# Performance work log

Hardware: AMD Instinct MI355X
Metric: run time of the kernel (lower is better)

## Reference

```python
import jax, jax.numpy as jnp
import numpy as np

DIM = 128      # d_msa
HEADS = 8
DH = 64        # dim_head
INNER = HEADS * DH  # 512
R = 64         # tie_attn_dim (MSA rows)
N = 512        # residues
DPAIR = 128
LN_EPS = 1e-5


def _layernorm(x, g, b):
    mu = jnp.mean(x, axis=-1, keepdims=True)
    var = jnp.mean((x - mu) ** 2, axis=-1, keepdims=True)
    return (x - mu) * jax.lax.rsqrt(var + LN_EPS) * g + b


def setup_inputs() -> dict:
    key = jax.random.key(0)
    ks = jax.random.split(key, 12)
    s = 0.02
    return {
        "x": jax.random.normal(ks[0], (R, N, DIM), jnp.float32),
        "pair_bias": jax.random.normal(ks[1], (1, N, N, DPAIR), jnp.float32),
        "Wq": jax.random.normal(ks[2], (DIM, INNER), jnp.float32) * s,
        "Wkv": jax.random.normal(ks[3], (DIM, 2 * INNER), jnp.float32) * s,
        "Wo": jax.random.normal(ks[4], (INNER, DIM), jnp.float32) * s,
        "bo": jnp.zeros((DIM,), jnp.float32),
        "ln_g": jnp.ones((DPAIR,), jnp.float32),
        "ln_b": jnp.zeros((DPAIR,), jnp.float32),
        "Wpair": jax.random.normal(ks[5], (DPAIR, HEADS), jnp.float32) * s,
        "Wsq": jax.random.normal(ks[6], (DIM, DIM), jnp.float32) * s,
        "bsq": jnp.zeros((DIM,), jnp.float32),
        "Wsk": jax.random.normal(ks[7], (DIM, DIM), jnp.float32) * s,
        "bsk": jnp.zeros((DIM,), jnp.float32),
        "tie_attn_dim": R,
    }


def reference(x, pair_bias, Wq, Wkv, Wo, bo, ln_g, ln_b, Wpair, Wsq, bsq, Wsk, bsk, tie_attn_dim):
    r = tie_attn_dim
    br, n, dim = x.shape
    b = br // r
    h, dh = HEADS, DH
    dsw = dim // h  # per-head dim inside PositionalWiseWeight

    # projections: (b*r, n, inner) -> (b, r, h, n, dh)
    q = (x @ Wq).reshape(b, r, n, h, dh).transpose(0, 1, 3, 2, 4)
    kv = x @ Wkv
    k, v = jnp.split(kv, 2, axis=-1)
    k = k.reshape(b, r, n, h, dh).transpose(0, 1, 3, 2, 4)
    v = v.reshape(b, r, n, h, dh).transpose(0, 1, 3, 2, 4)

    # soft tied row weights (PositionalWiseWeight): w[b, i(pos), h, r]
    m = x.reshape(b, r, n, dim)
    sq = (m[:, :1] @ Wsq + bsq).reshape(b, 1, n, h, dsw).transpose(0, 2, 3, 1, 4)  # b n h 1 d
    sk = (m @ Wsk + bsk).reshape(b, r, n, h, dsw).transpose(0, 2, 3, 1, 4)          # b n h r d
    wlog = jnp.einsum('bnhud,bnhrd->bnhr', sq, sk) / np.float32(np.sqrt(dsw))
    w = jax.nn.softmax(wlog, axis=-1)  # softmax over rows r

    # tied-row attention logits with soft weights
    scale = np.float32(dh) ** -0.5
    dots = jnp.einsum('bihr,brhid,brhjd->bhij', w, q, k) * scale

    # pair bias: LayerNorm + Linear(dim_pair -> heads), broadcast into logits
    pb = _layernorm(pair_bias, ln_g, ln_b) @ Wpair  # (b, i, j, h)
    dots = dots + pb.transpose(0, 3, 1, 2)

    attn = jax.nn.softmax(dots, axis=-1)  # (b, h, i, j)

    out = jnp.einsum('bhij,brhjd->brhid', attn, v)           # (b, r, h, n, dh)
    out = out.transpose(0, 1, 3, 2, 4).reshape(br, n, h * dh)
    out = out @ Wo + bo                                       # (b*r, n, dim)
    return out.reshape(1, br, n, dim)
```

## Files before the change

kernel.cpp:

```cpp
#include <hip/hip_runtime.h>
#include <hip/hip_bf16.h>

typedef unsigned short u16;
typedef unsigned int u32;
typedef __attribute__((ext_vector_type(8))) short short8;
typedef __attribute__((ext_vector_type(4))) float floatx4;

__device__ inline float bf2f(u16 u) { union { u32 i; float f; } v; v.i = ((u32)u) << 16; return v.f; }
__device__ inline u16 f2bf(float f) {
    union { float f; u32 i; } v; v.f = f;
    u32 lsb = (v.i >> 16) & 1u;
    v.i += 0x7fffu + lsb;
    return (u16)(v.i >> 16);
}

__device__ inline uint4 pack8(float4 a, float4 b) {
    uint4 q;
    q.x = (u32)f2bf(a.x) | ((u32)f2bf(a.y) << 16);
    q.y = (u32)f2bf(a.z) | ((u32)f2bf(a.w) << 16);
    q.z = (u32)f2bf(b.x) | ((u32)f2bf(b.y) << 16);
    q.w = (u32)f2bf(b.z) | ((u32)f2bf(b.w) << 16);
    return q;
}

__device__ inline void ld8(u16* dst, const float* src) {
    const float4 a = *(const float4*)src;
    const float4 b = *(const float4*)(src + 4);
    *(uint4*)dst = pack8(a, b);
}

__device__ inline void async16(u16* ldst, const u16* gsrc) {
    __builtin_amdgcn_global_load_lds((const __attribute__((address_space(1))) u32*)gsrc,
                                     (__attribute__((address_space(3))) u32*)ldst, 16, 0, 0);
}

template <int BM, int BN, class Epi>
__global__ __launch_bounds__(256) void gemm_nt(const u16* __restrict__ A, const u16* __restrict__ B,
                                               long sAz, long sBz, int lda, int ldb, int K, int zlog, Epi epi)
{
    constexpr int AELE = BM * 32, BELE = BN * 32;
    constexpr int IA = BM / 64, IB = BN / 64;
    constexpr bool STAGE = Epi::chunked;
    static_assert(!STAGE || BN == 128, "chunked epilogue assumes BN=128");
    constexpr int LDC = BN + 4;
    constexpr size_t OPB = sizeof(u16) * 2 * (AELE + BELE);
    constexpr size_t STB = STAGE ? sizeof(float) * (size_t)BM * LDC : 0;
    constexpr size_t LB = OPB > STB ? OPB : STB;
    __shared__ __align__(16) char smem[LB];
    u16* lds = (u16*)smem;
    const int tid  = threadIdx.x;
    const int lane = tid & 63;
    const int wave = tid >> 6;
    const int z    = blockIdx.z;
    const int zh   = z >> zlog;
    const int zk   = z & ((1 << zlog) - 1);
    const long row0 = (long)blockIdx.y * BM;
    const long col0 = (long)blockIdx.x * BN;
    const u16* Ab = A + (long)zh * sAz + row0 * lda + (long)zk * K;
    const u16* Bb = B + (long)zh * sBz + col0 * ldb + (long)zk * K;
    constexpr int WM = BM / 2, WN = BN / 2, TM = WM / 16, TN = WN / 16;
    const int wm = (wave >> 1) * WM;
    const int wn = (wave & 1) * WN;
    const int l15 = lane & 15;
    const int quad = lane >> 4;
    const int swz = (l15 >> 1) & 3;

    floatx4 acc[TM][TN];
#pragma unroll
    for (int i = 0; i < TM; i++)
#pragma unroll
        for (int j = 0; j < TN; j++) acc[i][j] = (floatx4){0.f, 0.f, 0.f, 0.f};

    auto stage = [&](int buf, int k0) {
        u16* base = lds + buf * (AELE + BELE);
#pragma unroll
        for (int i = 0; i < IA; i++) {
            int s = wave * (IA * 64) + i * 64 + lane;
            int r = s >> 2, c = (s & 3) ^ ((r >> 1) & 3);
            async16(base + (wave * (IA * 64) + i * 64) * 8, Ab + (long)r * lda + k0 + c * 8);
        }
        u16* bbase = base + AELE;
#pragma unroll
        for (int i = 0; i < IB; i++) {
            int s = wave * (IB * 64) + i * 64 + lane;
            int r = s >> 2, c = (s & 3) ^ ((r >> 1) & 3);
            async16(bbase + (wave * (IB * 64) + i * 64) * 8, Bb + (long)r * ldb + k0 + c * 8);
        }
    };

    stage(0, 0);
    const int nIter = K >> 5;
    for (int ki = 0; ki < nIter; ki++) {
        const int cur = ki & 1;
        __syncthreads();
        if (ki + 1 < nIter) stage(1 - cur, (ki + 1) << 5);
        const u16* As = lds + cur * (AELE + BELE);
        const u16* Bs = As + AELE;
        short8 af[TM], bfr[TN];
#pragma unroll
        for (int t = 0; t < TM; t++)
            af[t] = *(const short8*)(As + (wm + t * 16 + l15) * 32 + (quad ^ swz) * 8);
#pragma unroll
        for (int t = 0; t < TN; t++)
            bfr[t] = *(const short8*)(Bs + (wn + t * 16 + l15) * 32 + (quad ^ swz) * 8);
#pragma unroll
        for (int i = 0; i < TM; i++)
#pragma unroll
            for (int j = 0; j < TN; j++)
                acc[i][j] = __builtin_amdgcn_mfma_f32_16x16x32_bf16(af[i], bfr[j], acc[i][j], 0, 0, 0);
    }

    if constexpr (STAGE) {
        __syncthreads();
        float* cs = (float*)smem;
#pragma unroll
        for (int i = 0; i < TM; i++)
#pragma unroll
            for (int j = 0; j < TN; j++)
#pragma unroll
                for (int r = 0; r < 4; r++)
                    cs[(wm + i * 16 + quad * 4 + r) * LDC + (wn + j * 16 + l15)] = acc[i][j][r];
        __syncthreads();
        constexpr int CPT = (BM * BN) / (256 * 8);
#pragma unroll
        for (int k = 0; k < CPT; k++) {
            int g = k * 256 + tid;
            int row = g >> 4;
            int c8 = (g & 15) * 8;
            const float* p = cs + row * LDC + c8;
            float4 a = *(const float4*)p;
            float4 b = *(const float4*)(p + 4);
            epi.chunk(zh, zk, (int)row0 + row, (int)col0 + c8, a, b);
        }
    } else {
#pragma unroll
        for (int i = 0; i < TM; i++)
#pragma unroll
            for (int j = 0; j < TN; j++)
#pragma unroll
                for (int r = 0; r < 4; r++) {
                    int row = (int)row0 + wm + i * 16 + quad * 4 + r;
                    int col = (int)col0 + wn + j * 16 + l15;
                    epi(zh, zk, row, col, acc[i][j][r]);
                }
    }
}

struct EpiBiasBF {
    static constexpr bool chunked = true;
    u16* C; const float* bias; int ldc;
    __device__ void chunk(int, int, int row, int col, float4 a, float4 b) const {
        const float4* bp = (const float4*)(bias + col);
        float4 b0 = bp[0], b1 = bp[1];
        a.x += b0.x; a.y += b0.y; a.z += b0.z; a.w += b0.w;
        b.x += b1.x; b.y += b1.y; b.z += b1.z; b.w += b1.w;
        *(uint4*)(C + (long)row * ldc + col) = pack8(a, b);
    }
};
struct EpiQ {
    static constexpr bool chunked = true;
    u16* Qw; const float* w;
    __device__ void chunk(int, int, int row, int col, float4 a, float4 b) const {
        int r = row >> 9, i = row & 511, h = col >> 6, d = col & 63;
        float s = w[((long)(i * 8 + h)) * 64 + r] * 0.125f;
        a.x *= s; a.y *= s; a.z *= s; a.w *= s;
        b.x *= s; b.y *= s; b.z *= s; b.w *= s;
        *(uint4*)(Qw + (long)h * 2097152 + (long)i * 4096 + r * 64 + d) = pack8(a, b);
    }
};
struct EpiKV {
    static constexpr bool chunked = true;
    u16* Kp; u16* Vp;
    __device__ void chunk(int, int, int row, int col, float4 a, float4 b) const {
        int r = row >> 9, j = row & 511;
        u16* dst = (col < 512) ? Kp : Vp;
        int c = col & 511;
        int h = c >> 6, d = c & 63;
        *(uint4*)(dst + (long)h * 2097152 + (long)j * 4096 + r * 64 + d) = pack8(a, b);
    }
};
struct EpiDotsAtomic {
    static constexpr bool chunked = false;
    float* pbdots;
    __device__ void operator()(int zh, int, int row, int col, float v) const {
        atomicAdd(pbdots + (long)zh * 262144 + (long)row * 512 + col, v);
    }
};
struct EpiDotsPart {
    static constexpr bool chunked = false;
    float* pbd; float* parts;
    __device__ void operator()(int zh, int zk, int row, int col, float v) const {
        long idx = (long)zh * 262144 + (long)row * 512 + col;
        if (zk == 0) pbd[idx] += v;
        else         parts[(long)(zk - 1) * 2097152 + idx] = v;
    }
};
struct EpiPV {
    static constexpr bool chunked = true;
    u16* O2;
    __device__ void chunk(int zh, int, int row, int col, float4 a, float4 b) const {
        int r = col >> 6, d = col & 63;
        *(uint4*)(O2 + ((long)r * 512 + row) * 512 + zh * 64 + d) = pack8(a, b);
    }
};
struct EpiOut {
    static constexpr bool chunked = true;
    float* out; const float* bo;
    __device__ void chunk(int, int, int row, int col, float4 a, float4 b) const {
        const float4* bp = (const float4*)(bo + col);
        float4 b0 = bp[0], b1 = bp[1];
        a.x += b0.x; a.y += b0.y; a.z += b0.z; a.w += b0.w;
        b.x += b1.x; b.y += b1.y; b.z += b1.z; b.w += b1.w;
        float4* o = (float4*)(out + (long)row * 128 + col);
        o[0] = a; o[1] = b;
    }
};

__global__ __launch_bounds__(256) void f2bf_kernel(const float* __restrict__ src, u16* __restrict__ dst)
{
    long i = ((long)blockIdx.x * 256 + threadIdx.x) * 8;
    ld8(dst + i, src + i);
}

__global__ __launch_bounds__(256) void transpose_to_bf16(const float* __restrict__ src, u16* __restrict__ dst,
                                                         int R, int C)
{
    __shared__ u16 t[32][33];
    int c0 = blockIdx.x * 32, r0 = blockIdx.y * 32;
    int tx = threadIdx.x, ty = threadIdx.y;
#pragma unroll
    for (int i = 0; i < 32; i += 8) t[ty + i][tx] = f2bf(src[(long)(r0 + ty + i) * C + c0 + tx]);
    __syncthreads();
#pragma unroll
    for (int i = 0; i < 32; i += 8) dst[(long)(c0 + ty + i) * R + r0 + tx] = t[tx][ty + i];
}

__global__ __launch_bounds__(256) void transpose64(const u16* __restrict__ src, u16* __restrict__ dst,
                                                   long ss, long ds, int R, int C)
{
    __shared__ __align__(16) u16 t[64][72];
    const u16* s = src + (long)blockIdx.z * ss;
    u16* d = dst + (long)blockIdx.z * ds;
    int c0 = blockIdx.x * 64, r0 = blockIdx.y * 64;
    int tid = threadIdx.x;
    int row = tid >> 3, ch = tid & 7;
#pragma unroll
    for (int p = 0; p < 2; p++) {
        int r = row + p * 32;
        *(uint4*)&t[r][ch * 8] = *(const uint4*)(s + (long)(r0 + r) * C + c0 + ch * 8);
    }
    __syncthreads();
#pragma unroll
    for (int p = 0; p < 2; p++) {
        int cc = row + p * 32;
        u16 tmp[8];
#pragma unroll
        for (int j = 0; j < 8; j++) tmp[j] = t[ch * 8 + j][cc];
        *(uint4*)(d + (long)(c0 + cc) * R + r0 + ch * 8) = *(uint4*)tmp;
    }
}

__global__ __launch_bounds__(256) void rowweight_kernel(const u16* __restrict__ sk, const u16* __restrict__ sq,
                                                        float* __restrict__ w)
{
    int wid = blockIdx.x * 4 + (threadIdx.x >> 6);
    int lane = threadIdx.x & 63;
    int i = wid >> 3, h = wid & 7;
    const u16* sqp = sq + i * 128 + h * 16;
    const u16* skp = sk + ((long)lane * 512 + i) * 128 + h * 16;
    float dot = 0.f;
#pragma unroll
    for (int c = 0; c < 16; c++) dot += bf2f(sqp[c]) * bf2f(skp[c]);
    float logit = dot * 0.25f;
    float m = logit;
#pragma unroll
    for (int o = 32; o > 0; o >>= 1) m = fmaxf(m, __shfl_xor(m, o));
    float e = __expf(logit - m);
    float ssum = e;
#pragma unroll
    for (int o = 32; o > 0; o >>= 1) ssum += __shfl_xor(ssum, o);
    w[(long)wid * 64 + lane] = e / ssum;
}

__global__ __launch_bounds__(256) void pbprep_kernel(const float* __restrict__ g, const float* __restrict__ b,
                                                     const float* __restrict__ Wp, float* __restrict__ Wg,
                                                     float* __restrict__ SB)
{
    int tid = threadIdx.x;
    for (int t = tid; t < 1024; t += 256) Wg[t] = g[t >> 3] * Wp[t];
    if (tid < 16) {
        int h = tid & 7;
        const float* src = (tid < 8) ? g : b;
        float s = 0.f;
        for (int c = 0; c < 128; c++) s += src[c] * Wp[c * 8 + h];
        SB[tid] = s;
    }
}

__global__ __launch_bounds__(256) void pb_kernel(const float* __restrict__ pair, const float* __restrict__ Wg,
                                                 const float* __restrict__ SB, float* __restrict__ pb)
{
    __shared__ __align__(16) float Ls[64 * 132];
    __shared__ float sWg[1024];
    __shared__ float sSB[16];
    int tid = threadIdx.x;
    for (int t = tid; t < 1024; t += 256) sWg[t] = Wg[t];
    if (tid < 16) sSB[tid] = SB[tid];
    long base = (long)blockIdx.x * 8192;
    const float4* src = (const float4*)(pair + base);
#pragma unroll
    for (int k = 0; k < 8; k++) {
        int e = tid + k * 256;
        float4 v = src[e];
        int r = e >> 5, c = (e & 31) << 2;
        *(float4*)(&Ls[r * 132 + c]) = v;
    }
    __syncthreads();
    int r = tid >> 2, sub = tid & 3;
    const float* row = &Ls[r * 132];
    float sum = 0.f, sqs = 0.f;
#pragma unroll
    for (int k = 0; k < 8; k++) {
        float4 v = *(const float4*)(&row[sub * 32 + k * 4]);
        sum += v.x + v.y + v.z + v.w;
        sqs += v.x * v.x + v.y * v.y + v.z * v.z + v.w * v.w;
    }
    sum += __shfl_xor(sum, 1); sqs += __shfl_xor(sqs, 1);
    sum += __shfl_xor(sum, 2); sqs += __shfl_xor(sqs, 2);
    float mu = sum * (1.f / 128.f);
    float var = sqs * (1.f / 128.f) - mu * mu;
    float rstd = rsqrtf(var + 1e-5f);
    int h0 = sub * 2;
    float a0 = 0.f, a1 = 0.f;
#pragma unroll
    for (int k = 0; k < 32; k++) {
        float4 v = *(const float4*)(&row[k * 4]);
        int c = k * 4;
        a0 += v.x * sWg[c * 8 + h0]     + v.y * sWg[(c + 1) * 8 + h0]
            + v.z * sWg[(c + 2) * 8 + h0] + v.w * sWg[(c + 3) * 8 + h0];
        a1 += v.x * sWg[c * 8 + h0 + 1]     + v.y * sWg[(c + 1) * 8 + h0 + 1]
            + v.z * sWg[(c + 2) * 8 + h0 + 1] + v.w * sWg[(c + 3) * 8 + h0 + 1];
    }
    long idx = (long)blockIdx.x * 64 + r;
    pb[(long)h0 * 262144 + idx]       = rstd * (a0 - mu * sSB[h0])     + sSB[8 + h0];
    pb[(long)(h0 + 1) * 262144 + idx] = rstd * (a1 - mu * sSB[h0 + 1]) + sSB[8 + h0 + 1];
}

__global__ __launch_bounds__(256) void softmax_kernel(const float* __restrict__ dots,
                                                      const float* __restrict__ parts, int np,
                                                      u16* __restrict__ attn)
{
    int row = blockIdx.x * 4 + (threadIdx.x >> 6);
    int lane = threadIdx.x & 63;
    long base = (long)row * 512;
    const float* dp = dots + base;
    float v[8];
#pragma unroll
    for (int k = 0; k < 8; k++) v[k] = dp[k * 64 + lane];
    for (int t = 0; t < np; t++) {
        const float* pp = parts + (long)t * 2097152 + base;
#pragma unroll
        for (int k = 0; k < 8; k++) v[k] += pp[k * 64 + lane];
    }
    float m = v[0];
#pragma unroll
    for (int k = 1; k < 8; k++) m = fmaxf(m, v[k]);
#pragma unroll
    for (int o = 32; o > 0; o >>= 1) m = fmaxf(m, __shfl_xor(m, o));
    float s = 0.f;
#pragma unroll
    for (int k = 0; k < 8; k++) { v[k] = __expf(v[k] - m); s += v[k]; }
#pragma unroll
    for (int o = 32; o > 0; o >>= 1) s += __shfl_xor(s, o);
    float inv = 1.f / s;
    u16* ap = attn + (long)row * 512;
#pragma unroll
    for (int k = 0; k < 8; k++) ap[k * 64 + lane] = f2bf(v[k] * inv);
}

extern "C" void kernel_launch(void* const* d_in, const int* in_sizes, int n_in,
                              void* d_out, int out_size, void* d_ws, size_t ws_size,
                              hipStream_t stream)
{
    const float* x    = (const float*)d_in[0];
    const float* pair = (const float*)d_in[1];
    const float* Wq   = (const float*)d_in[2];
    const float* Wkv  = (const float*)d_in[3];
    const float* Wo   = (const float*)d_in[4];
    const float* bo   = (const float*)d_in[5];
    const float* lng  = (const float*)d_in[6];
    const float* lnb  = (const float*)d_in[7];
    const float* Wp   = (const float*)d_in[8];
    const float* Wsq  = (const float*)d_in[9];
    const float* bsq  = (const float*)d_in[10];
    const float* Wsk  = (const float*)d_in[11];
    const float* bsk  = (const float*)d_in[12];
    float* out = (float*)d_out;

    char* ws = (char*)d_ws;
    size_t off = 0;
    auto alloc = [&](size_t bytes) -> char* {
        char* p = ws + off; off += (bytes + 255) & ~(size_t)255; return p;
    };
    u16* WqT  = (u16*)alloc(512 * 128 * 2);
    u16* WkvT = (u16*)alloc(1024 * 128 * 2);
    u16* WskT = (u16*)alloc(128 * 128 * 2);
    u16* WsqT = (u16*)alloc(128 * 128 * 2);
    u16* WoT  = (u16*)alloc(128 * 512 * 2);
    u16* xbf  = (u16*)alloc((size_t)32768 * 128 * 2);
    u16* sk   = (u16*)alloc((size_t)32768 * 128 * 2);
    u16* sq   = (u16*)alloc(512 * 128 * 2);
    float* w  = (float*)alloc((size_t)4096 * 64 * 4);
    float* Wg = (float*)alloc(1024 * 4);
    float* SB = (float*)alloc(16 * 4);
    u16* bufA = (u16*)alloc((size_t)8 * 512 * 4096 * 2);
    u16* bufB = (u16*)alloc((size_t)8 * 512 * 4096 * 2);
    u16* Vt   = (u16*)alloc((size_t)8 * 4096 * 512 * 2);
    float* pbd = (float*)alloc((size_t)8 * 512 * 512 * 4);
    float* parts = (float*)alloc((size_t)3 * 2097152 * 4);
    const bool useParts = (off <= ws_size);
    u16* attn = sk;

    dim3 blk(256);
    dim3 tb(32, 8);

    f2bf_kernel<<<dim3(2048), blk, 0, stream>>>(x, xbf);
    pbprep_kernel<<<dim3(1), blk, 0, stream>>>(lng, lnb, Wp, Wg, SB);

    transpose_to_bf16<<<dim3(16, 4, 1), tb, 0, stream>>>(Wq,  WqT,  128, 512);
    transpose_to_bf16<<<dim3(32, 4, 1), tb, 0, stream>>>(Wkv, WkvT, 128, 1024);
    transpose_to_bf16<<<dim3(4, 4, 1),  tb, 0, stream>>>(Wsk, WskT, 128, 128);
    transpose_to_bf16<<<dim3(4, 4, 1),  tb, 0, stream>>>(Wsq, WsqT, 128, 128);
    transpose_to_bf16<<<dim3(4, 16, 1), tb, 0, stream>>>(Wo,  WoT,  512, 128);

    gemm_nt<64, 128, EpiBiasBF><<<dim3(1, 512, 1), blk, 0, stream>>>(
        xbf, WskT, 0, 0, 128, 128, 128, 0, EpiBiasBF{sk, bsk, 128});
    gemm_nt<64, 128, EpiBiasBF><<<dim3(1, 8, 1), blk, 0, stream>>>(
        xbf, WsqT, 0, 0, 128, 128, 128, 0, EpiBiasBF{sq, bsq, 128});
    rowweight_kernel<<<dim3(1024), blk, 0, stream>>>(sk, sq, w);

    gemm_nt<128, 128, EpiKV><<<dim3(8, 256, 1), blk, 0, stream>>>(
        xbf, WkvT, 0, 0, 128, 128, 128, 0, EpiKV{bufB, bufA});
    transpose64<<<dim3(64, 8, 8), blk, 0, stream>>>(bufA, Vt, 2097152, 2097152, 512, 4096);

    gemm_nt<128, 128, EpiQ><<<dim3(4, 256, 1), blk, 0, stream>>>(
        xbf, WqT, 0, 0, 128, 128, 128, 0, EpiQ{bufA, w});

    pb_kernel<<<dim3(4096), blk, 0, stream>>>(pair, Wg, SB, pbd);

    if (useParts) {
        gemm_nt<128, 128, EpiDotsPart><<<dim3(4, 4, 32), blk, 0, stream>>>(
            bufA, bufB, 2097152, 2097152, 4096, 4096, 1024, 2, EpiDotsPart{pbd, parts});
        softmax_kernel<<<dim3(1024), blk, 0, stream>>>(pbd, parts, 3, attn);
    } else {
        gemm_nt<128, 128, EpiDotsAtomic><<<dim3(4, 4, 64), blk, 0, stream>>>(
            bufA, bufB, 2097152, 2097152, 4096, 4096, 512, 3, EpiDotsAtomic{pbd});
        softmax_kernel<<<dim3(1024), blk, 0, stream>>>(pbd, pbd, 0, attn);
    }

    gemm_nt<128, 128, EpiPV><<<dim3(32, 4, 8), blk, 0, stream>>>(
        attn, Vt, 262144, 2097152, 512, 512, 512, 0, EpiPV{bufB});

    gemm_nt<64, 128, EpiOut><<<dim3(1, 512, 1), blk, 0, stream>>>(
        bufB, WoT, 0, 0, 512, 512, 512, 0, EpiOut{out, bo});
}
```

Measured before the change: 421.0 us.

## Use 4-slot LDS pipeline with explicit vmcnt waits and chunked epilogue staging

Replaces the double-buffered K loop in the generic GEMM with a 4-slot ring that keeps two K-tiles of async global-to-LDS loads in flight. Each step waits with explicit vmcnt counts and a single raw barrier instead of __syncthreads, so load latency can hide behind the MFMA work. The staged epilogue now writes 64 rows at a time, which keeps the LDS footprint near the larger ring buffer, and the pair-bias kernel launch moves ahead of the Q projection. The risks are the hand-written wait counts and a possible loss of occupancy from the larger LDS allocation.

```diff
diff --git a/kernel.cpp b/kernel.cpp
--- a/kernel.cpp
+++ b/kernel.cpp
@@ -34,18 +34,37 @@
                                      (__attribute__((address_space(3))) u32*)ldst, 16, 0, 0);
 }
 
+template <int N> __device__ inline void waitvm() {
+    static_assert(N == 0 || N == 3 || N == 4 || N == 6 || N == 8, "unsupported vmcnt");
+    if constexpr (N == 0) asm volatile("s_waitcnt vmcnt(0)" ::: "memory");
+    if constexpr (N == 3) asm volatile("s_waitcnt vmcnt(3)" ::: "memory");
+    if constexpr (N == 4) asm volatile("s_waitcnt vmcnt(4)" ::: "memory");
+    if constexpr (N == 6) asm volatile("s_waitcnt vmcnt(6)" ::: "memory");
+    if constexpr (N == 8) asm volatile("s_waitcnt vmcnt(8)" ::: "memory");
+}
+__device__ inline void barrier_raw() {
+    asm volatile("s_barrier" ::: "memory");
+    __builtin_amdgcn_sched_barrier(0);
+}
+__device__ inline void waitlgkm0() {
+    asm volatile("s_waitcnt lgkmcnt(0)" ::: "memory");
+    __builtin_amdgcn_sched_barrier(0);
+}
+
 template <int BM, int BN, class Epi>
 __global__ __launch_bounds__(256) void gemm_nt(const u16* __restrict__ A, const u16* __restrict__ B,
                                                long sAz, long sBz, int lda, int ldb, int K, int zlog, Epi epi)
 {
     constexpr int AELE = BM * 32, BELE = BN * 32;
+    constexpr int SLOT = AELE + BELE;
     constexpr int IA = BM / 64, IB = BN / 64;
+    constexpr int PW = IA + IB;
     constexpr bool STAGE = Epi::chunked;
     static_assert(!STAGE || BN == 128, "chunked epilogue assumes BN=128");
     constexpr int LDC = BN + 4;
-    constexpr size_t OPB = sizeof(u16) * 2 * (AELE + BELE);
-    constexpr size_t STB = STAGE ? sizeof(float) * (size_t)BM * LDC : 0;
-    constexpr size_t LB = OPB > STB ? OPB : STB;
+    constexpr size_t RB = sizeof(u16) * 4 * (size_t)SLOT;
+    constexpr size_t EB = STAGE ? sizeof(float) * 64 * (size_t)LDC : 0;
+    constexpr size_t LB = RB > EB ? RB : EB;
     __shared__ __align__(16) char smem[LB];
     u16* lds = (u16*)smem;
     const int tid  = threadIdx.x;
@@ -71,30 +90,26 @@
 #pragma unroll
         for (int j = 0; j < TN; j++) acc[i][j] = (floatx4){0.f, 0.f, 0.f, 0.f};
 
-    auto stage = [&](int buf, int k0) {
-        u16* base = lds + buf * (AELE + BELE);
-#pragma unroll
-        for (int i = 0; i < IA; i++) {
-            int s = wave * (IA * 64) + i * 64 + lane;
+    auto stage = [&](int slot, int ki) {
+        const int k0 = ki << 5;
+        u16* base = lds + slot * SLOT;
+#pragma unroll
+        for (int i2 = 0; i2 < IA; i2++) {
+            int s = wave * (IA * 64) + i2 * 64 + lane;
             int r = s >> 2, c = (s & 3) ^ ((r >> 1) & 3);
-            async16(base + (wave * (IA * 64) + i * 64) * 8, Ab + (long)r * lda + k0 + c * 8);
+            async16(base + (wave * (IA * 64) + i2 * 64) * 8, Ab + (long)r * lda + k0 + c * 8);
         }
         u16* bbase = base + AELE;
 #pragma unroll
-        for (int i = 0; i < IB; i++) {
-            int s = wave * (IB * 64) + i * 64 + lane;
+        for (int i2 = 0; i2 < IB; i2++) {
+            int s = wave * (IB * 64) + i2 * 64 + lane;
             int r = s >> 2, c = (s & 3) ^ ((r >> 1) & 3);
-            async16(bbase + (wave * (IB * 64) + i * 64) * 8, Bb + (long)r * ldb + k0 + c * 8);
+            async16(bbase + (wave * (IB * 64) + i2 * 64) * 8, Bb + (long)r * ldb + k0 + c * 8);
         }
     };
 
-    stage(0, 0);
-    const int nIter = K >> 5;
-    for (int ki = 0; ki < nIter; ki++) {
-        const int cur = ki & 1;
-        __syncthreads();
-        if (ki + 1 < nIter) stage(1 - cur, (ki + 1) << 5);
-        const u16* As = lds + cur * (AELE + BELE);
+    auto compute = [&](int slot) {
+        const u16* As = lds + slot * SLOT;
         const u16* Bs = As + AELE;
         short8 af[TM], bfr[TN];
 #pragma unroll
@@ -103,34 +118,53 @@
 #pragma unroll
         for (int t = 0; t < TN; t++)
             bfr[t] = *(const short8*)(Bs + (wn + t * 16 + l15) * 32 + (quad ^ swz) * 8);
+        waitlgkm0();
 #pragma unroll
         for (int i = 0; i < TM; i++)
 #pragma unroll
             for (int j = 0; j < TN; j++)
                 acc[i][j] = __builtin_amdgcn_mfma_f32_16x16x32_bf16(af[i], bfr[j], acc[i][j], 0, 0, 0);
-    }
+    };
+
+    const int nIter = K >> 5;
+    stage(0, 0);
+    stage(1, 1);
+    for (int i = 0; i + 2 < nIter; i++) {
+        stage((i + 2) & 3, i + 2);
+        waitvm<2 * PW>();
+        barrier_raw();
+        compute(i & 3);
+    }
+    waitvm<PW>(); barrier_raw(); compute((nIter - 2) & 3);
+    waitvm<0>();  barrier_raw(); compute((nIter - 1) & 3);
 
     if constexpr (STAGE) {
-        __syncthreads();
         float* cs = (float*)smem;
-#pragma unroll
-        for (int i = 0; i < TM; i++)
-#pragma unroll
-            for (int j = 0; j < TN; j++)
-#pragma unroll
-                for (int r = 0; r < 4; r++)
-                    cs[(wm + i * 16 + quad * 4 + r) * LDC + (wn + j * 16 + l15)] = acc[i][j][r];
-        __syncthreads();
-        constexpr int CPT = (BM * BN) / (256 * 8);
-#pragma unroll
-        for (int k = 0; k < CPT; k++) {
-            int g = k * 256 + tid;
-            int row = g >> 4;
-            int c8 = (g & 15) * 8;
-            const float* p = cs + row * LDC + c8;
-            float4 a = *(const float4*)p;
-            float4 b = *(const float4*)(p + 4);
-            epi.chunk(zh, zk, (int)row0 + row, (int)col0 + c8, a, b);
+        constexpr int NP = BM / 64;
+#pragma unroll
+        for (int p = 0; p < NP; p++) {
+            __syncthreads();
+            if ((wm >> 6) == p) {
+                const int lr0 = wm & 63;
+#pragma unroll
+                for (int i = 0; i < TM; i++)
+#pragma unroll
+                    for (int j = 0; j < TN; j++)
+#pragma unroll
+                        for (int r = 0; r < 4; r++)
+                            cs[(lr0 + i * 16 + quad * 4 + r) * LDC + wn + j * 16 + l15] = acc[i][j][r];
+            }
+            __syncthreads();
+            constexpr int CPT = (64 * BN) / (256 * 8);
+#pragma unroll
+            for (int k = 0; k < CPT; k++) {
+                int g = k * 256 + tid;
+                int row = g >> 4, c8 = (g & 15) * 8;
+                const float* pp = cs + row * LDC + c8;
+                float4 a = *(const float4*)pp;
+                float4 b = *(const float4*)(pp + 4);
+                epi.chunk(zh, zk, (int)row0 + p * 64 + row, (int)col0 + c8, a, b);
+            }
         }
     } else {
 #pragma unroll
@@ -443,10 +477,10 @@
         xbf, WkvT, 0, 0, 128, 128, 128, 0, EpiKV{bufB, bufA});
     transpose64<<<dim3(64, 8, 8), blk, 0, stream>>>(bufA, Vt, 2097152, 2097152, 512, 4096);
 
+    pb_kernel<<<dim3(4096), blk, 0, stream>>>(pair, Wg, SB, pbd);
+
     gemm_nt<128, 128, EpiQ><<<dim3(4, 256, 1), blk, 0, stream>>>(
         xbf, WqT, 0, 0, 128, 128, 128, 0, EpiQ{bufA, w});
-
-    pb_kernel<<<dim3(4096), blk, 0, stream>>>(pair, Wg, SB, pbd);
 
     if (useParts) {
         gemm_nt<128, 128, EpiDotsPart><<<dim3(4, 4, 32), blk, 0, stream>>>(
```

Result: no change. 418.2 us (-0.7%).
